# Kernel tuning notes

Hardware: AMD Instinct MI355X
Metric: run time of the kernel (lower is better)

Reference implementation:

```python
import jax, jax.numpy as jnp
import numpy as np
import math

N_BLOCKS, DEPTH, K = 5, 10, 2


def build_dilations():
    # Mirrors WaveNet.__init__: list of (new_dilation, init_dilation) per layer.
    dil = []
    init = 1
    for _ in range(N_BLOCKS):
        new = 1
        for _ in range(DEPTH):
            dil.append((new, init))
            init = new
            new *= 2
    return dil


def conv1d_k2(x, w):
    # x: [N, Cin, L], w: [Cout, Cin, 2]; VALID conv -> [N, Cout, L-1]
    return jax.lax.conv_general_dilated(x, w, (1,), 'VALID',
                                        dimension_numbers=('NCH', 'OIH', 'NCH'))


def pw(x, w):
    # 1x1 conv: x [N, Cin, L], w [Cout, Cin]
    return jnp.einsum('oi,nil->nol', w, x)


def dilate(x, dilation, init_dilation):
    # Faithful port of the pytorch-wavenet dilate(): refolds time into batch.
    # All shape arithmetic is static Python ints (jit-safe).
    r = dilation / init_dilation
    if r == 1:
        return x
    n, c, l = x.shape
    new_l = int(math.ceil(l / r) * r)
    if new_l != l:
        x = jnp.pad(x, ((0, 0), (0, 0), (new_l - l, 0)))  # pad_start with zeros
        l = new_l
    l_new = int(round(l * init_dilation / dilation))
    n_new = int(round(n * dilation / init_dilation))
    x = jnp.transpose(x, (1, 2, 0)).reshape(c, l_new, n_new)  # (c, l, n) row-major view
    return jnp.transpose(x, (2, 0, 1))


def wavenet_forward(tokens, emb, pre_w, filt_w, gate_w, res_w, skip_w,
                    post_w1, post_b1, post_w2, post_b2):
    # preprocess: embedding -> [B, C_res, L], then causal k=2 conv (length preserved)
    x = jnp.transpose(emb[tokens], (0, 2, 1))
    x = conv1d_k2(jnp.pad(x, ((0, 0), (0, 0), (K - 1, 0))), pre_w)
    skip = None
    for i, (d, init_d) in enumerate(build_dilations()):
        xd = dilate(x, d, init_d)                       # fold/unfold to dilation d
        z = jnp.tanh(conv1d_k2(xd, filt_w[i])) * jax.nn.sigmoid(conv1d_k2(xd, gate_w[i]))
        s = pw(dilate(z, 1, d), skip_w[i])              # skip contribution, unfolded
        x = pw(z, res_w[i]) + xd[:, :, K - 1:]          # residual connection (folded)
        skip = s if skip is None else skip[:, :, -s.shape[2]:] + s
    h = jax.nn.relu(skip)
    h = jax.nn.relu(pw(h, post_w1) + post_b1[None, :, None])
    return pw(h, post_w2) + post_b2[None, :, None]


def setup_inputs() -> dict:
    key = jax.random.key(0)
    ks = jax.random.split(key, 11)
    B, L = 4, 8192
    V, Cr, Cd, Cs, Ce = 256, 32, 32, 512, 256
    NL = N_BLOCKS * DEPTH
    f = lambda k, shape: jax.random.normal(k, shape, jnp.float32) * 0.1
    return {
        'tokens': jax.random.randint(ks[0], (B, L), 0, V, dtype=jnp.int32),
        'emb': f(ks[1], (V, Cr)),
        'pre_w': f(ks[2], (Cr, Cr, K)),
        'filt_w': f(ks[3], (NL, Cd, Cr, K)),
        'gate_w': f(ks[4], (NL, Cd, Cr, K)),
        'res_w': f(ks[5], (NL, Cr, Cd)),
        'skip_w': f(ks[6], (NL, Cs, Cd)),
        'post_w1': f(ks[7], (Ce, Cs)),
        'post_b1': f(ks[8], (Ce,)),
        'post_w2': f(ks[9], (V, Ce)),
        'post_b2': f(ks[10], (V,)),
    }


def reference(tokens, emb, pre_w, filt_w, gate_w, res_w, skip_w,
              post_w1, post_b1, post_w2, post_b2):
    return wavenet_forward(tokens, emb, pre_w, filt_w, gate_w, res_w, skip_w,
                           post_w1, post_b1, post_w2, post_b2)
```

## Files before the change

kernel.cpp:

```cpp
#include <hip/hip_runtime.h>
#include <math.h>

#define NB 4
#define L0 8192
#define CR 32
#define CD 32
#define CS 512
#define CE 256
#define NV 256
#define OUT_T 5632
#define XSTRIDE 8192
#define NL 50
#define KCAT 1600
#define TW 128

typedef __attribute__((ext_vector_type(8))) short  short8;
typedef __attribute__((ext_vector_type(4))) float  f32x4;
typedef __attribute__((ext_vector_type(4))) float  f4;
typedef __attribute__((ext_vector_type(4))) unsigned short us4;

static __device__ __forceinline__ unsigned short f2bf(float f) {
    unsigned int u = __builtin_bit_cast(unsigned int, f);
    u = (u + 0x7FFFu + ((u >> 16) & 1u)) >> 16;
    return (unsigned short)u;
}

__global__ __launch_bounds__(256) void k_prep(const float* __restrict__ sw,
                                              const float* __restrict__ w1,
                                              const float* __restrict__ w2,
                                              unsigned short* __restrict__ wsb,
                                              unsigned short* __restrict__ w1b,
                                              unsigned short* __restrict__ w2b)
{
    int idx = blockIdx.x * 256 + threadIdx.x;
    if (idx < NL * CS * CD) {
        int l = idx >> 14;
        int co = (idx >> 5) & 511;
        int c = idx & 31;
        wsb[co * KCAT + l * 32 + c] = f2bf(sw[idx]);
    } else if (idx < NL * CS * CD + CE * CS) {
        int e = idx - NL * CS * CD;
        w1b[e] = f2bf(w1[e]);
    } else {
        int e = idx - NL * CS * CD - CE * CS;
        w2b[e] = f2bf(w2[e]);
    }
}

__global__ __launch_bounds__(256) void k_pre(const int* __restrict__ tokens,
                                             const float* __restrict__ emb,
                                             const float* __restrict__ pw,
                                             float* __restrict__ x)
{
    int idx = blockIdx.x * 256 + threadIdx.x;
    int t = idx & (L0 - 1);
    int o = (idx >> 13) & 31;
    int b = idx >> 18;
    const int* tb = tokens + b * L0;
    const float* e1 = emb + tb[t] * CR;
    const float* w = pw + o * CR * 2;
    float acc = 0.f;
    if (t > 0) {
        const float* e0 = emb + tb[t - 1] * CR;
#pragma unroll
        for (int i = 0; i < CR; ++i)
            acc += w[i * 2] * e0[i] + w[i * 2 + 1] * e1[i];
    } else {
#pragma unroll
        for (int i = 0; i < CR; ++i)
            acc += w[i * 2 + 1] * e1[i];
    }
    x[(b * CR + o) * XSTRIDE + t] = acc;
}

struct PairSmem {
    float T00[32][136];
    float T01[32][136];
    float T10[32][136];
    float T11[32][136];
    float ZA[32][136];
    float ZB[32][136];
    float wfT[64][33];
    float wgT[64][33];
    float rwT[32][33];
    unsigned short ZsT[2][128][32];
};
static_assert(sizeof(PairSmem) <= 160 * 1024, "LDS overflow");

static __device__ __forceinline__ void gate_tile(
    const float (*__restrict__ X0)[136], const float (*__restrict__ X1)[136],
    float (*__restrict__ Zf)[136], unsigned short (*__restrict__ Zb)[32],
    const float (*__restrict__ wf)[33], const float (*__restrict__ wg)[33],
    int c, int j0)
{
    float af[8] = {0, 0, 0, 0, 0, 0, 0, 0};
    float ag[8] = {0, 0, 0, 0, 0, 0, 0, 0};
#pragma unroll
    for (int i = 0; i < 32; ++i) {
        float av[8], bv[8];
        *(f4*)&av[0] = *(const f4*)&X0[i][j0];
        *(f4*)&av[4] = *(const f4*)&X0[i][j0 + 4];
        *(f4*)&bv[0] = *(const f4*)&X1[i][j0];
        *(f4*)&bv[4] = *(const f4*)&X1[i][j0 + 4];
        float f0 = wf[2 * i][c], f1 = wf[2 * i + 1][c];
        float g0 = wg[2 * i][c], g1 = wg[2 * i + 1][c];
#pragma unroll
        for (int k = 0; k < 8; ++k) {
            af[k] += f0 * av[k] + f1 * bv[k];
            ag[k] += g0 * av[k] + g1 * bv[k];
        }
    }
#pragma unroll
    for (int k = 0; k < 8; ++k) {
        float e2a = __expf(2.f * af[k]);
        float th = 1.f - __fdividef(2.f, e2a + 1.f);
        float sg = __fdividef(1.f, 1.f + __expf(-ag[k]));
        float z = th * sg;
        Zf[c][j0 + k] = z;
        Zb[j0 + k][c] = f2bf(z);
    }
}

static __device__ __forceinline__ void resid_tile(
    const float (*__restrict__ Xd)[136], const float (*__restrict__ Zf)[136],
    const float (*__restrict__ rw)[33], float* __restrict__ out, int ch, int j0)
{
    *(f4*)&out[0] = *(const f4*)&Xd[ch][j0];
    *(f4*)&out[4] = *(const f4*)&Xd[ch][j0 + 4];
#pragma unroll
    for (int i = 0; i < 32; ++i) {
        float w = rw[i][ch];
        float zv[8];
        *(f4*)&zv[0] = *(const f4*)&Zf[i][j0];
        *(f4*)&zv[4] = *(const f4*)&Zf[i][j0 + 4];
#pragma unroll
        for (int k = 0; k < 8; ++k)
            out[k] += w * zv[k];
    }
}

__global__ __launch_bounds__(512, 1) void k_pair(
    const float* __restrict__ x0, float* __restrict__ x_out,
    unsigned short* __restrict__ Zt,
    const float* __restrict__ fw1, const float* __restrict__ gw1,
    const float* __restrict__ rw1,
    const float* __restrict__ fw2, const float* __restrict__ gw2,
    const float* __restrict__ rw2,
    int T0, int T1, int T2, int d1, int d2, int P1, int P2,
    int skip1, int skip2, int kOff1, int kOff2)
{
    extern __shared__ char smraw[];
    PairSmem& sm = *reinterpret_cast<PairSmem*>(smraw);
    const int tid = threadIdx.x;
    const int b = blockIdx.y;
    const int t0 = blockIdx.x * TW;
    const int baseA = t0 - P2;
    const int baseB = t0 + d2 - P2;

    for (int e = tid; e < 2048; e += 512) {
        int c = e >> 6, i2 = e & 63;
        sm.wfT[i2][c] = fw1[e];
        sm.wgT[i2][c] = gw1[e];
    }
    for (int e = tid; e < 1024; e += 512)
        sm.rwT[e & 31][e >> 5] = rw1[e];
    {
        int ch = tid >> 4;
        int j0 = (tid & 15) * 8;
        const float* row = x0 + ((size_t)b * CR + ch) * XSTRIDE;
        const int bases[4] = {baseA, baseA + d1, baseB, baseB + d1};
        float* const dsts[4] = {&sm.T00[ch][j0], &sm.T01[ch][j0],
                                &sm.T10[ch][j0], &sm.T11[ch][j0]};
#pragma unroll
        for (int q = 0; q < 4; ++q) {
            int iu0 = bases[q] + j0 - P1;
            float v[8];
            if (iu0 >= 0 && iu0 + 7 < T0) {
#pragma unroll
                for (int k = 0; k < 8; ++k) v[k] = row[iu0 + k];
            } else {
#pragma unroll
                for (int k = 0; k < 8; ++k) {
                    int iu = iu0 + k;
                    v[k] = (iu >= 0 && iu < T0) ? row[iu] : 0.f;
                }
            }
#pragma unroll
            for (int k = 0; k < 8; ++k) dsts[q][k] = v[k];
        }
    }
    __syncthreads();

    {
        int c = tid & 31;
        int j0 = (tid >> 5) * 8;
        gate_tile(sm.T00, sm.T01, sm.ZA, sm.ZsT[0], sm.wfT, sm.wgT, c, j0);
        gate_tile(sm.T10, sm.T11, sm.ZB, sm.ZsT[1], sm.wfT, sm.wgT, c, j0);
    }
    __syncthreads();

    for (int e = tid; e < 2048; e += 512) {
        int c = e >> 6, i2 = e & 63;
        sm.wfT[i2][c] = fw2[e];
        sm.wgT[i2][c] = gw2[e];
    }
#pragma unroll
    for (int s = 0; s < 2; ++s) {
        int lin = tid + s * 512;
        int tile = lin >> 9;
        int r = lin & 511;
        int j = r >> 2, cq = (r & 3) * 8;
        int u = (tile ? baseB : baseA) + j;
        if (u >= skip1 && u < T1) {
            unsigned short* dst =
                Zt + ((size_t)b * OUT_T + (u - skip1)) * KCAT + kOff1 + cq;
            *(short8*)dst = *(const short8*)&sm.ZsT[tile][j][cq];
        }
    }
    {
        int ch = tid >> 4;
        int j0 = (tid & 15) * 8;
        float acc[8];
        resid_tile(sm.T01, sm.ZA, sm.rwT, acc, ch, j0);
#pragma unroll
        for (int k = 0; k < 8; ++k)
            sm.T00[ch][j0 + k] = (t0 + j0 + k >= P2) ? acc[k] : 0.f;
        resid_tile(sm.T11, sm.ZB, sm.rwT, acc, ch, j0);
#pragma unroll
        for (int k = 0; k < 8; ++k)
            sm.T10[ch][j0 + k] = acc[k];
    }
    __syncthreads();

    for (int e = tid; e < 1024; e += 512)
        sm.rwT[e & 31][e >> 5] = rw2[e];
    {
        int c = tid & 31;
        int j0 = (tid >> 5) * 8;
        gate_tile(sm.T00, sm.T10, sm.ZA, sm.ZsT[0], sm.wfT, sm.wgT, c, j0);
    }
    __syncthreads();

    {
        int j = tid >> 2, cq = (tid & 3) * 8;
        int t = t0 + j;
        if (t >= skip2 && t < T2) {
            unsigned short* dst =
                Zt + ((size_t)b * OUT_T + (t - skip2)) * KCAT + kOff2 + cq;
            *(short8*)dst = *(const short8*)&sm.ZsT[0][j][cq];
        }
    }
    {
        int ch = tid >> 4;
        int j0 = (tid & 15) * 8;
        float acc[8];
        resid_tile(sm.T10, sm.ZA, sm.rwT, acc, ch, j0);
        float* orow = x_out + ((size_t)b * CR + ch) * XSTRIDE;
#pragma unroll
        for (int k = 0; k < 8; ++k) {
            int t = t0 + j0 + k;
            if (t < T2) orow[t] = acc[k];
        }
    }
}

template <int MODE>
__global__ __launch_bounds__(256) void k_gemm(
    const unsigned short* __restrict__ A,
    const unsigned short* __restrict__ B,
    const float* __restrict__ bias,
    void* __restrict__ Cout, int M, int K)
{
    __shared__ unsigned short Asm[128][72];
    __shared__ unsigned short Bsm[64][72];
    const int tid = threadIdx.x;
    const int n0 = blockIdx.x * 64;
    const int m0 = blockIdx.y * 128;
    const int b = blockIdx.z;
    const unsigned short* Bb = B + (size_t)b * OUT_T * K;
    const int lane = tid & 63;
    const int wm = tid >> 6;
    f32x4 acc[2][4];
#pragma unroll
    for (int fm = 0; fm < 2; ++fm)
#pragma unroll
        for (int fn = 0; fn < 4; ++fn)
            acc[fm][fn] = (f32x4){0.f, 0.f, 0.f, 0.f};

    for (int kb = 0; kb < K; kb += 64) {
        __syncthreads();
#pragma unroll
        for (int it = 0; it < 4; ++it) {
            int lin = tid + it * 256;
            int row = lin >> 3, c8 = (lin & 7) * 8;
            *(short8*)&Asm[row][c8] =
                *(const short8*)&A[(size_t)(m0 + row) * K + kb + c8];
        }
#pragma unroll
        for (int it = 0; it < 2; ++it) {
            int lin = tid + it * 256;
            int row = lin >> 3, c8 = (lin & 7) * 8;
            *(short8*)&Bsm[row][c8] =
                *(const short8*)&Bb[(size_t)(n0 + row) * K + kb + c8];
        }
        __syncthreads();
#pragma unroll
        for (int kk = 0; kk < 2; ++kk) {
            short8 a[2], bb[4];
#pragma unroll
            for (int fm = 0; fm < 2; ++fm)
                a[fm] = *(const short8*)&Asm[wm * 32 + fm * 16 + (lane & 15)]
                                           [kk * 32 + (lane >> 4) * 8];
#pragma unroll
            for (int fn = 0; fn < 4; ++fn)
                bb[fn] = *(const short8*)&Bsm[fn * 16 + (lane & 15)]
                                            [kk * 32 + (lane >> 4) * 8];
#pragma unroll
            for (int fm = 0; fm < 2; ++fm)
#pragma unroll
                for (int fn = 0; fn < 4; ++fn)
                    acc[fm][fn] = __builtin_amdgcn_mfma_f32_16x16x32_bf16(
                        a[fm], bb[fn], acc[fm][fn], 0, 0, 0);
        }
    }
#pragma unroll
    for (int fm = 0; fm < 2; ++fm) {
        int mb = m0 + wm * 32 + fm * 16 + (lane >> 4) * 4;
#pragma unroll
        for (int fn = 0; fn < 4; ++fn) {
            int n = n0 + fn * 16 + (lane & 15);
            float v[4];
#pragma unroll
            for (int r = 0; r < 4; ++r) {
                v[r] = acc[fm][fn][r];
                if (MODE >= 1) v[r] += bias[mb + r];
                if (MODE <= 1) v[r] = v[r] > 0.f ? v[r] : 0.f;
            }
            if (MODE == 2) {
                float* o = (float*)Cout;
#pragma unroll
                for (int r = 0; r < 4; ++r)
                    o[((size_t)b * NV + mb + r) * OUT_T + n] = v[r];
            } else {
                unsigned short* o = (unsigned short*)Cout;
                us4 pk;
#pragma unroll
                for (int r = 0; r < 4; ++r) pk[r] = f2bf(v[r]);
                *(us4*)&o[((size_t)b * OUT_T + n) * M + mb] = pk;
            }
        }
    }
}

extern "C" void kernel_launch(void* const* d_in, const int* in_sizes, int n_in,
                              void* d_out, int out_size, void* d_ws, size_t ws_size,
                              hipStream_t stream)
{
    const int*   tokens  = (const int*)d_in[0];
    const float* emb     = (const float*)d_in[1];
    const float* pre_w   = (const float*)d_in[2];
    const float* filt_w  = (const float*)d_in[3];
    const float* gate_w  = (const float*)d_in[4];
    const float* res_w   = (const float*)d_in[5];
    const float* skip_w  = (const float*)d_in[6];
    const float* post_w1 = (const float*)d_in[7];
    const float* post_b1 = (const float*)d_in[8];
    const float* post_w2 = (const float*)d_in[9];
    const float* post_b2 = (const float*)d_in[10];
    float* out = (float*)d_out;

    char* ws = (char*)d_ws;
    float* xA = (float*)ws;                 ws += (size_t)NB * CR * XSTRIDE * 4;
    float* xB = (float*)ws;                 ws += (size_t)NB * CR * XSTRIDE * 4;
    unsigned short* Zt    = (unsigned short*)ws; ws += (size_t)NB * OUT_T * KCAT * 2;
    unsigned short* skipT = (unsigned short*)ws; ws += (size_t)NB * OUT_T * CS * 2;
    unsigned short* h1T   = (unsigned short*)ws; ws += (size_t)NB * OUT_T * CE * 2;
    unsigned short* wsb   = (unsigned short*)ws; ws += (size_t)CS * KCAT * 2;
    unsigned short* w1b   = (unsigned short*)ws; ws += (size_t)CE * CS * 2;
    unsigned short* w2b   = (unsigned short*)ws; ws += (size_t)NV * CE * 2;

    k_prep<<<3968, 256, 0, stream>>>(skip_w, post_w1, post_w2, wsb, w1b, w2b);
    k_pre<<<(NB * CR * L0) / 256, 256, 0, stream>>>(tokens, emb, pre_w, xA);

    int dArr[NL], pArr[NL], tArr[NL];
    {
        int T = L0, init = 1, li = 0;
        for (int blk = 0; blk < 5; ++blk) {
            int nw = 1;
            for (int j = 0; j < 10; ++j) {
                int d = nw, P = 0;
                if (d > init) {
                    int r = d / init;
                    int l = T / init;
                    int nl = ((l + r - 1) / r) * r;
                    P = (nl - l) * init;
                }
                int T_out = T + P - d;
                dArr[li] = d; pArr[li] = P; tArr[li] = T_out;
                T = T_out; init = d; nw <<= 1; ++li;
            }
        }
    }

    float* xin = xA;
    float* xout = xB;
    for (int p = 0; p < 25; ++p) {
        int l1 = 2 * p, l2 = 2 * p + 1;
        int T0 = (l1 == 0) ? L0 : tArr[l1 - 1];
        int T1 = tArr[l1], T2 = tArr[l2];
        int ntiles = (T2 + TW - 1) / TW;
        dim3 grid(ntiles, NB);
        k_pair<<<grid, 512, sizeof(PairSmem), stream>>>(
            xin, xout, Zt,
            filt_w + (size_t)l1 * CD * CR * 2,
            gate_w + (size_t)l1 * CD * CR * 2,
            res_w + (size_t)l1 * CR * CD,
            filt_w + (size_t)l2 * CD * CR * 2,
            gate_w + (size_t)l2 * CD * CR * 2,
            res_w + (size_t)l2 * CR * CD,
            T0, T1, T2, dArr[l1], dArr[l2], pArr[l1], pArr[l2],
            T1 - OUT_T, T2 - OUT_T, l1 * 32, l2 * 32);
        float* tmp = xin; xin = xout; xout = tmp;
    }

    dim3 gs(OUT_T / 64, CS / 128, NB);
    k_gemm<0><<<gs, 256, 0, stream>>>(wsb, Zt, nullptr, skipT, CS, KCAT);
    dim3 g1(OUT_T / 64, CE / 128, NB);
    k_gemm<1><<<g1, 256, 0, stream>>>(w1b, skipT, post_b1, h1T, CE, CS);
    dim3 g2(OUT_T / 64, NV / 128, NB);
    k_gemm<2><<<g2, 256, 0, stream>>>(w2b, h1T, post_b2, out, NV, CE);
}
```

Measured before the change: 1.642 ms.

## Halve pair-kernel tile to 64 with 256 threads and widen GEMM N-tile to 128

The fused dilated-layer pair kernel now uses 64-wide time tiles with 256 threads. A compact LDS layout drops the separate bf16 transposed Z buffer, and the bf16 packing into Zt is done directly from the fp32 Z tile at store time. The smaller LDS footprint and block size are meant to let several blocks share a CU and to launch more blocks per layer, improving occupancy. The skip/post GEMMs switch to 128x128 tiles for more MFMA work per load, at the cost of more accumulator registers and fewer blocks. The Zt stores now gather strided LDS reads, and halo reloads grow relative to the smaller tile.

Result: faster. 1.544 ms (-6.0%).

```diff
diff --git a/kernel.cpp b/kernel.cpp
--- a/kernel.cpp
+++ b/kernel.cpp
@@ -12,7 +12,7 @@
 #define XSTRIDE 8192
 #define NL 50
 #define KCAT 1600
-#define TW 128
+#define TW 64
 
 typedef __attribute__((ext_vector_type(8))) short  short8;
 typedef __attribute__((ext_vector_type(4))) float  f32x4;
@@ -73,23 +73,17 @@
     x[(b * CR + o) * XSTRIDE + t] = acc;
 }
 
-struct PairSmem {
-    float T00[32][136];
-    float T01[32][136];
-    float T10[32][136];
-    float T11[32][136];
-    float ZA[32][136];
-    float ZB[32][136];
+struct PairSmem2 {
+    float X[4][32][68];
+    float Z[2][32][68];
     float wfT[64][33];
     float wgT[64][33];
     float rwT[32][33];
-    unsigned short ZsT[2][128][32];
 };
-static_assert(sizeof(PairSmem) <= 160 * 1024, "LDS overflow");
-
-static __device__ __forceinline__ void gate_tile(
-    const float (*__restrict__ X0)[136], const float (*__restrict__ X1)[136],
-    float (*__restrict__ Zf)[136], unsigned short (*__restrict__ Zb)[32],
+
+static __device__ __forceinline__ void gate_tile2(
+    const float (*__restrict__ X0)[68], const float (*__restrict__ X1)[68],
+    float (*__restrict__ Zf)[68],
     const float (*__restrict__ wf)[33], const float (*__restrict__ wg)[33],
     int c, int j0)
 {
@@ -115,31 +109,26 @@
         float e2a = __expf(2.f * af[k]);
         float th = 1.f - __fdividef(2.f, e2a + 1.f);
         float sg = __fdividef(1.f, 1.f + __expf(-ag[k]));
-        float z = th * sg;
-        Zf[c][j0 + k] = z;
-        Zb[j0 + k][c] = f2bf(z);
-    }
-}
-
-static __device__ __forceinline__ void resid_tile(
-    const float (*__restrict__ Xd)[136], const float (*__restrict__ Zf)[136],
-    const float (*__restrict__ rw)[33], float* __restrict__ out, int ch, int j0)
-{
-    *(f4*)&out[0] = *(const f4*)&Xd[ch][j0];
-    *(f4*)&out[4] = *(const f4*)&Xd[ch][j0 + 4];
-#pragma unroll
-    for (int i = 0; i < 32; ++i) {
-        float w = rw[i][ch];
-        float zv[8];
-        *(f4*)&zv[0] = *(const f4*)&Zf[i][j0];
-        *(f4*)&zv[4] = *(const f4*)&Zf[i][j0 + 4];
-#pragma unroll
-        for (int k = 0; k < 8; ++k)
-            out[k] += w * zv[k];
-    }
-}
-
-__global__ __launch_bounds__(512, 1) void k_pair(
+        Zf[c][j0 + k] = th * sg;
+    }
+}
+
+static __device__ __forceinline__ void zt_store(
+    const float (*__restrict__ Zf)[68], unsigned short* __restrict__ Zt,
+    int b, int tl, int cq, int u, int skipO, int Tlim, int kOff)
+{
+    if (u >= skipO && u < Tlim) {
+        short8 pk;
+#pragma unroll
+        for (int q = 0; q < 8; ++q)
+            pk[q] = (short)f2bf(Zf[cq + q][tl]);
+        unsigned short* dst =
+            Zt + ((size_t)b * OUT_T + (u - skipO)) * KCAT + kOff + cq;
+        *(short8*)dst = pk;
+    }
+}
+
+__global__ __launch_bounds__(256) void k_pair(
     const float* __restrict__ x0, float* __restrict__ x_out,
     unsigned short* __restrict__ Zt,
     const float* __restrict__ fw1, const float* __restrict__ gw1,
@@ -150,27 +139,25 @@
     int skip1, int skip2, int kOff1, int kOff2)
 {
     extern __shared__ char smraw[];
-    PairSmem& sm = *reinterpret_cast<PairSmem*>(smraw);
+    PairSmem2& sm = *reinterpret_cast<PairSmem2*>(smraw);
     const int tid = threadIdx.x;
     const int b = blockIdx.y;
     const int t0 = blockIdx.x * TW;
     const int baseA = t0 - P2;
     const int baseB = t0 + d2 - P2;
 
-    for (int e = tid; e < 2048; e += 512) {
+    for (int e = tid; e < 2048; e += 256) {
         int c = e >> 6, i2 = e & 63;
         sm.wfT[i2][c] = fw1[e];
         sm.wgT[i2][c] = gw1[e];
     }
-    for (int e = tid; e < 1024; e += 512)
+    for (int e = tid; e < 1024; e += 256)
         sm.rwT[e & 31][e >> 5] = rw1[e];
     {
-        int ch = tid >> 4;
-        int j0 = (tid & 15) * 8;
+        int ch = tid >> 3;
+        int j0 = (tid & 7) * 8;
         const float* row = x0 + ((size_t)b * CR + ch) * XSTRIDE;
         const int bases[4] = {baseA, baseA + d1, baseB, baseB + d1};
-        float* const dsts[4] = {&sm.T00[ch][j0], &sm.T01[ch][j0],
-                                &sm.T10[ch][j0], &sm.T11[ch][j0]};
 #pragma unroll
         for (int q = 0; q < 4; ++q) {
             int iu0 = bases[q] + j0 - P1;
@@ -186,7 +173,7 @@
                 }
             }
 #pragma unroll
-            for (int k = 0; k < 8; ++k) dsts[q][k] = v[k];
+            for (int k = 0; k < 8; ++k) sm.X[q][ch][j0 + k] = v[k];
         }
     }
     __syncthreads();
@@ -194,67 +181,82 @@
     {
         int c = tid & 31;
         int j0 = (tid >> 5) * 8;
-        gate_tile(sm.T00, sm.T01, sm.ZA, sm.ZsT[0], sm.wfT, sm.wgT, c, j0);
-        gate_tile(sm.T10, sm.T11, sm.ZB, sm.ZsT[1], sm.wfT, sm.wgT, c, j0);
+        gate_tile2(sm.X[0], sm.X[1], sm.Z[0], sm.wfT, sm.wgT, c, j0);
+        gate_tile2(sm.X[2], sm.X[3], sm.Z[1], sm.wfT, sm.wgT, c, j0);
     }
     __syncthreads();
 
-    for (int e = tid; e < 2048; e += 512) {
+    for (int e = tid; e < 2048; e += 256) {
         int c = e >> 6, i2 = e & 63;
         sm.wfT[i2][c] = fw2[e];
         sm.wgT[i2][c] = gw2[e];
     }
-#pragma unroll
-    for (int s = 0; s < 2; ++s) {
-        int lin = tid + s * 512;
-        int tile = lin >> 9;
-        int r = lin & 511;
-        int j = r >> 2, cq = (r & 3) * 8;
-        int u = (tile ? baseB : baseA) + j;
-        if (u >= skip1 && u < T1) {
-            unsigned short* dst =
-                Zt + ((size_t)b * OUT_T + (u - skip1)) * KCAT + kOff1 + cq;
-            *(short8*)dst = *(const short8*)&sm.ZsT[tile][j][cq];
-        }
-    }
-    {
-        int ch = tid >> 4;
-        int j0 = (tid & 15) * 8;
-        float acc[8];
-        resid_tile(sm.T01, sm.ZA, sm.rwT, acc, ch, j0);
-#pragma unroll
-        for (int k = 0; k < 8; ++k)
-            sm.T00[ch][j0 + k] = (t0 + j0 + k >= P2) ? acc[k] : 0.f;
-        resid_tile(sm.T11, sm.ZB, sm.rwT, acc, ch, j0);
-#pragma unroll
-        for (int k = 0; k < 8; ++k)
-            sm.T10[ch][j0 + k] = acc[k];
+    {
+        int tl = tid >> 2;
+        int cq = (tid & 3) * 8;
+        zt_store(sm.Z[0], Zt, b, tl, cq, baseA + tl, skip1, T1, kOff1);
+        zt_store(sm.Z[1], Zt, b, tl, cq, baseB + tl, skip1, T1, kOff1);
+    }
+    {
+        int ch = tid >> 3;
+        int j0 = (tid & 7) * 8;
+        float accA[8], accB[8];
+        *(f4*)&accA[0] = *(const f4*)&sm.X[1][ch][j0];
+        *(f4*)&accA[4] = *(const f4*)&sm.X[1][ch][j0 + 4];
+        *(f4*)&accB[0] = *(const f4*)&sm.X[3][ch][j0];
+        *(f4*)&accB[4] = *(const f4*)&sm.X[3][ch][j0 + 4];
+#pragma unroll
+        for (int i = 0; i < 32; ++i) {
+            float w = sm.rwT[i][ch];
+            float za[8], zb[8];
+            *(f4*)&za[0] = *(const f4*)&sm.Z[0][i][j0];
+            *(f4*)&za[4] = *(const f4*)&sm.Z[0][i][j0 + 4];
+            *(f4*)&zb[0] = *(const f4*)&sm.Z[1][i][j0];
+            *(f4*)&zb[4] = *(const f4*)&sm.Z[1][i][j0 + 4];
+#pragma unroll
+            for (int k = 0; k < 8; ++k) {
+                accA[k] += w * za[k];
+                accB[k] += w * zb[k];
+            }
+        }
+#pragma unroll
+        for (int k = 0; k < 8; ++k) {
+            sm.X[0][ch][j0 + k] = (t0 + j0 + k >= P2) ? accA[k] : 0.f;
+            sm.X[2][ch][j0 + k] = accB[k];
+        }
     }
     __syncthreads();
 
-    for (int e = tid; e < 1024; e += 512)
+    for (int e = tid; e < 1024; e += 256)
         sm.rwT[e & 31][e >> 5] = rw2[e];
     {
         int c = tid & 31;
         int j0 = (tid >> 5) * 8;
-        gate_tile(sm.T00, sm.T10, sm.ZA, sm.ZsT[0], sm.wfT, sm.wgT, c, j0);
+        gate_tile2(sm.X[0], sm.X[2], sm.Z[0], sm.wfT, sm.wgT, c, j0);
     }
     __syncthreads();
 
     {
-        int j = tid >> 2, cq = (tid & 3) * 8;
-        int t = t0 + j;
-        if (t >= skip2 && t < T2) {
-            unsigned short* dst =
-                Zt + ((size_t)b * OUT_T + (t - skip2)) * KCAT + kOff2 + cq;
-            *(short8*)dst = *(const short8*)&sm.ZsT[0][j][cq];
-        }
-    }
-    {
-        int ch = tid >> 4;
-        int j0 = (tid & 15) * 8;
+        int tl = tid >> 2;
+        int cq = (tid & 3) * 8;
+        zt_store(sm.Z[0], Zt, b, tl, cq, t0 + tl, skip2, T2, kOff2);
+    }
+    {
+        int ch = tid >> 3;
+        int j0 = (tid & 7) * 8;
         float acc[8];
-        resid_tile(sm.T10, sm.ZA, sm.rwT, acc, ch, j0);
+        *(f4*)&acc[0] = *(const f4*)&sm.X[2][ch][j0];
+        *(f4*)&acc[4] = *(const f4*)&sm.X[2][ch][j0 + 4];
+#pragma unroll
+        for (int i = 0; i < 32; ++i) {
+            float w = sm.rwT[i][ch];
+            float zv[8];
+            *(f4*)&zv[0] = *(const f4*)&sm.Z[0][i][j0];
+            *(f4*)&zv[4] = *(const f4*)&sm.Z[0][i][j0 + 4];
+#pragma unroll
+            for (int k = 0; k < 8; ++k)
+                acc[k] += w * zv[k];
+        }
         float* orow = x_out + ((size_t)b * CR + ch) * XSTRIDE;
 #pragma unroll
         for (int k = 0; k < 8; ++k) {
@@ -272,19 +274,19 @@
     void* __restrict__ Cout, int M, int K)
 {
     __shared__ unsigned short Asm[128][72];
-    __shared__ unsigned short Bsm[64][72];
+    __shared__ unsigned short Bsm[128][72];
     const int tid = threadIdx.x;
-    const int n0 = blockIdx.x * 64;
+    const int n0 = blockIdx.x * 128;
     const int m0 = blockIdx.y * 128;
     const int b = blockIdx.z;
     const unsigned short* Bb = B + (size_t)b * OUT_T * K;
     const int lane = tid & 63;
     const int wm = tid >> 6;
-    f32x4 acc[2][4];
+    f32x4 acc[2][8];
 #pragma unroll
     for (int fm = 0; fm < 2; ++fm)
 #pragma unroll
-        for (int fn = 0; fn < 4; ++fn)
+        for (int fn = 0; fn < 8; ++fn)
             acc[fm][fn] = (f32x4){0.f, 0.f, 0.f, 0.f};
 
     for (int kb = 0; kb < K; kb += 64) {
@@ -297,7 +299,7 @@
                 *(const short8*)&A[(size_t)(m0 + row) * K + kb + c8];
         }
 #pragma unroll
-        for (int it = 0; it < 2; ++it) {
+        for (int it = 0; it < 4; ++it) {
             int lin = tid + it * 256;
             int row = lin >> 3, c8 = (lin & 7) * 8;
             *(short8*)&Bsm[row][c8] =
@@ -306,19 +308,19 @@
         __syncthreads();
 #pragma unroll
         for (int kk = 0; kk < 2; ++kk) {
-            short8 a[2], bb[4];
+            short8 a[2], bb[8];
 #pragma unroll
             for (int fm = 0; fm < 2; ++fm)
                 a[fm] = *(const short8*)&Asm[wm * 32 + fm * 16 + (lane & 15)]
                                            [kk * 32 + (lane >> 4) * 8];
 #pragma unroll
-            for (int fn = 0; fn < 4; ++fn)
+            for (int fn = 0; fn < 8; ++fn)
                 bb[fn] = *(const short8*)&Bsm[fn * 16 + (lane & 15)]
                                             [kk * 32 + (lane >> 4) * 8];
 #pragma unroll
             for (int fm = 0; fm < 2; ++fm)
 #pragma unroll
-                for (int fn = 0; fn < 4; ++fn)
+                for (int fn = 0; fn < 8; ++fn)
                     acc[fm][fn] = __builtin_amdgcn_mfma_f32_16x16x32_bf16(
                         a[fm], bb[fn], acc[fm][fn], 0, 0, 0);
         }
@@ -327,7 +329,7 @@
     for (int fm = 0; fm < 2; ++fm) {
         int mb = m0 + wm * 32 + fm * 16 + (lane >> 4) * 4;
 #pragma unroll
-        for (int fn = 0; fn < 4; ++fn) {
+        for (int fn = 0; fn < 8; ++fn) {
             int n = n0 + fn * 16 + (lane & 15);
             float v[4];
 #pragma unroll
@@ -410,7 +412,7 @@
         int T1 = tArr[l1], T2 = tArr[l2];
         int ntiles = (T2 + TW - 1) / TW;
         dim3 grid(ntiles, NB);
-        k_pair<<<grid, 512, sizeof(PairSmem), stream>>>(
+        k_pair<<<grid, 256, sizeof(PairSmem2), stream>>>(
             xin, xout, Zt,
             filt_w + (size_t)l1 * CD * CR * 2,
             gate_w + (size_t)l1 * CD * CR * 2,
@@ -423,10 +425,10 @@
         float* tmp = xin; xin = xout; xout = tmp;
     }
 
-    dim3 gs(OUT_T / 64, CS / 128, NB);
+    dim3 gs(OUT_T / 128, CS / 128, NB);
     k_gemm<0><<<gs, 256, 0, stream>>>(wsb, Zt, nullptr, skipT, CS, KCAT);
-    dim3 g1(OUT_T / 64, CE / 128, NB);
+    dim3 g1(OUT_T / 128, CE / 128, NB);
     k_gemm<1><<<g1, 256, 0, stream>>>(w1b, skipT, post_b1, h1T, CE, CS);
-    dim3 g2(OUT_T / 64, NV / 128, NB);
+    dim3 g2(OUT_T / 128, NV / 128, NB);
     k_gemm<2><<<g2, 256, 0, stream>>>(w2b, h1T, post_b2, out, NV, CE);
 }
```
